# Kernel tuning notes

Measured on AMD Instinct MI355X. Metric: run time of the kernel, lower is better.

## Reference

```python
import jax, jax.numpy as jnp
import numpy as np


def _sage_layer(x_src, x_dst, src, dst, n_dst, W_neigh, W_self, b):
    # mean aggregation of src features onto dst nodes (zero for isolated dst)
    msgs = x_src[src]                                            # [E, d_in]
    summed = jax.ops.segment_sum(msgs, dst, num_segments=n_dst)  # [n_dst, d_in]
    deg = jax.ops.segment_sum(jnp.ones_like(dst, dtype=x_src.dtype), dst,
                              num_segments=n_dst)                # [n_dst]
    mean = summed / jnp.maximum(deg, 1)[:, None]
    # DGL SAGEConv('mean'): fc_self(h_dst) + fc_neigh(h_mean) + bias
    return x_dst @ W_self + mean @ W_neigh + b


def setup_inputs() -> dict:
    key = jax.random.key(0)
    ks = jax.random.split(key, 12)
    N_SRC, D_IN, HID, OUT = 100000, 128, 256, 64
    SIZE1, SIZE2 = 25000, 5000
    E1, E2 = 800000, 160000

    def glorot(k, shape):
        lim = np.sqrt(6.0 / (shape[0] + shape[1])).astype(np.float32)
        return jax.random.uniform(k, shape, jnp.float32, -lim, lim)

    return {
        "x": jax.random.normal(ks[0], (N_SRC, D_IN), jnp.float32),
        "W_self1": glorot(ks[1], (D_IN, HID)),
        "W_neigh1": glorot(ks[2], (D_IN, HID)),
        "b1": jnp.zeros((HID,), jnp.float32),
        "W_self2": glorot(ks[3], (HID, OUT)),
        "W_neigh2": glorot(ks[4], (HID, OUT)),
        "b2": jnp.zeros((OUT,), jnp.float32),
        "edge_src1": jax.random.randint(ks[5], (E1,), 0, N_SRC, jnp.int32),
        "edge_dst1": jax.random.randint(ks[6], (E1,), 0, SIZE1, jnp.int32),
        "edge_src2": jax.random.randint(ks[7], (E2,), 0, SIZE1, jnp.int32),
        "edge_dst2": jax.random.randint(ks[8], (E2,), 0, SIZE2, jnp.int32),
        "size1": SIZE1,
        "size2": SIZE2,
    }


def reference(x, W_self1, W_neigh1, b1, W_self2, W_neigh2, b2,
              edge_src1, edge_dst1, edge_src2, edge_dst2, size1, size2):
    # Layer 1: src = all nodes, dst = first size1 nodes
    h = _sage_layer(x, x[:size1], edge_src1, edge_dst1, size1,
                    W_neigh1, W_self1, b1)
    h = jax.nn.relu(h)  # dropout is identity in eval mode
    # Layer 2: src = layer-1 outputs (size1 nodes), dst = first size2 nodes
    h = _sage_layer(h, h[:size2], edge_src2, edge_dst2, size2,
                    W_neigh2, W_self2, b2)
    return jax.nn.log_softmax(h, axis=-1)
```

## Files before the change

kernel.cpp:

```cpp
#include <hip/hip_runtime.h>


constexpr int D_IN  = 128;
constexpr int HID   = 256;
constexpr int OUT_D = 64;
constexpr int SIZE1 = 25000;
constexpr int SIZE2 = 5000;
constexpr int SEGC  = 16;
constexpr int OVFS  = 48;
constexpr int ROW   = 8 * SEGC + OVFS;
constexpr int ECH   = 2048;

using bf16x8 = __attribute__((ext_vector_type(8))) short;
using f32x4  = __attribute__((ext_vector_type(4))) float;
using f32x2  = __attribute__((ext_vector_type(2))) float;

__device__ inline unsigned short f32_to_bf16_rne(float f) {
    unsigned u = __builtin_bit_cast(unsigned, f);
    u = (u + 0x7fffu + ((u >> 16) & 1u)) >> 16;
    return (unsigned short)u;
}
__device__ inline unsigned pack_bf16(float lo, float hi) {
    return (unsigned)f32_to_bf16_rne(lo) | ((unsigned)f32_to_bf16_rne(hi) << 16);
}
__device__ inline void add16(float* a, uint4 v) {
    const unsigned u[4] = {v.x, v.y, v.z, v.w};
#pragma unroll
    for (int i = 0; i < 4; ++i) {
        f32x2 f0 = __builtin_amdgcn_cvt_pk_f32_fp8(u[i], false);
        f32x2 f1 = __builtin_amdgcn_cvt_pk_f32_fp8(u[i], true);
        a[i * 4 + 0] += f0.x; a[i * 4 + 1] += f0.y;
        a[i * 4 + 2] += f1.x; a[i * 4 + 3] += f1.y;
    }
}

__device__ inline void fill_body(const int* __restrict__ es,
                                 const int* __restrict__ ed, int E, int base0,
                                 int* __restrict__ cnt, int* __restrict__ ovf,
                                 int* __restrict__ csr) {
    int xcc;
    asm volatile("s_getreg_b32 %0, hwreg(HW_REG_XCC_ID)" : "=s"(xcc));
    xcc &= 7;
#pragma unroll
    for (int j = 0; j < ECH / 256; ++j) {
        int e = base0 + j * 256;
        if (e < E) {
            int d = ed[e];
            int pos = atomicAdd(&cnt[d * 8 + xcc], 1);
            if (pos < SEGC) {
                csr[(long)d * ROW + xcc * SEGC + pos] = es[e];
            } else {
                int po = atomicAdd(&ovf[d], 1);
                if (po < OVFS) csr[(long)d * ROW + 8 * SEGC + po] = es[e];
            }
        }
    }
}

__global__ void megafuse(const int* __restrict__ es1, const int* __restrict__ ed1,
                         int E1, int* __restrict__ cnt1, int* __restrict__ ovf1,
                         int* __restrict__ csr1,
                         const float* __restrict__ x, unsigned* __restrict__ xbu,
                         unsigned* __restrict__ x8u, long n4,
                         const float* __restrict__ Ws1, const float* __restrict__ Wn1,
                         const float* __restrict__ Ws2, const float* __restrict__ Wn2,
                         unsigned short* __restrict__ Wt1,
                         unsigned short* __restrict__ Wt2,
                         int f1, int f2) {
    const int b = blockIdx.x;
    const int tid = threadIdx.x;
    if (b < f1) {
        fill_body(es1, ed1, E1, b * ECH + tid, cnt1, ovf1, csr1);
    } else if (b < f2) {
        long i0 = (long)(b - f1) * 512 + tid;
#pragma unroll
        for (int j = 0; j < 2; ++j) {
            long i = i0 + j * 256;
            if (i < n4) {
                float4 v = reinterpret_cast<const float4*>(x)[i];
                int p = __builtin_amdgcn_cvt_pk_fp8_f32(v.x, v.y, 0, false);
                p = __builtin_amdgcn_cvt_pk_fp8_f32(v.z, v.w, p, true);
                x8u[i] = (unsigned)p;
                if (i < (long)SIZE1 * (D_IN / 4)) {
                    uint2 o;
                    o.x = pack_bf16(v.x, v.y);
                    o.y = pack_bf16(v.z, v.w);
                    reinterpret_cast<uint2*>(xbu)[i] = o;
                }
            }
        }
    } else {
        int i = (b - f2) * 256 + tid;
        if (i < HID * (2 * D_IN)) {
            int n = i >> 8, k = i & 255;
            float v = (k < D_IN) ? Ws1[k * HID + n] : Wn1[(k - D_IN) * HID + n];
            Wt1[i] = f32_to_bf16_rne(v);
        } else {
            int j = i - HID * (2 * D_IN);
            if (j < OUT_D * (2 * HID)) {
                int n = j >> 9, k = j & 511;
                float v = (k < HID) ? Ws2[k * OUT_D + n] : Wn2[(k - HID) * OUT_D + n];
                Wt2[j] = f32_to_bf16_rne(v);
            }
        }
    }
}

template <int GL, bool FUSE>
__global__ void agg_pull6(const uint4* __restrict__ X4,
                          const int* __restrict__ csr,
                          const int* __restrict__ cnt,
                          const int* __restrict__ ovf,
                          uint4* __restrict__ meanOut, int ndst, int aggBlocks,
                          const int* __restrict__ esF, const int* __restrict__ edF,
                          int EF, int* __restrict__ cntF, int* __restrict__ ovfF,
                          int* __restrict__ csrF) {
    if (FUSE && (int)blockIdx.x >= aggBlocks) {
        fill_body(esF, edF, EF, ((int)blockIdx.x - aggBlocks) * ECH + threadIdx.x,
                  cntF, ovfF, csrF);
        return;
    }
    constexpr int NG = 64 / GL;
    constexpr int NR = (64 + NG * 8 - 1) / (NG * 8);
    const int wid = threadIdx.x >> 6;
    const int lane = threadIdx.x & 63;
    const int d = blockIdx.x * 4 + wid;
    if (d >= ndst) return;

    int myc = 0;
    if (lane < 8) myc = min(cnt[d * 8 + lane], SEGC);
    else if (lane == 8) myc = min(ovf[d], OVFS);
    int cum[10];
    cum[0] = 0;
#pragma unroll
    for (int k = 0; k < 9; ++k) cum[k + 1] = cum[k] + __shfl(myc, k);
    const int n = cum[9];
    const long rowb = (long)d * ROW;

    int slot = lane;
#pragma unroll
    for (int t = 1; t < 9; ++t)
        if (lane >= cum[t]) slot = (t < 8 ? t * SEGC : 8 * SEGC) + (lane - cum[t]);
    int myidx = 0;
    if (lane < n) myidx = csr[rowb + slot];

    const int g = lane / GL;
    const int c = lane % GL;
    const int nmain = min(n, 64);

    float acc[16];
#pragma unroll
    for (int j = 0; j < 16; ++j) acc[j] = 0.0f;

#pragma unroll
    for (int r = 0; r < NR; ++r) {
        const int base = r * NG * 8;
        if (base < nmain) {
            int s[8];
            bool act[8];
#pragma unroll
            for (int t = 0; t < 8; ++t) {
                const int e = base + g + NG * t;
                int ss = __shfl(myidx, e & 63);
                act[t] = (e < nmain);
                s[t] = act[t] ? ss : 0;
            }
            uint4 v[8];
#pragma unroll
            for (int t = 0; t < 8; ++t) v[t] = X4[(long)s[t] * GL + c];
#pragma unroll
            for (int t = 0; t < 8; ++t)
                if (act[t]) add16(acc, v[t]);
        }
    }
    for (int j2 = 64 + g; j2 < n; j2 += NG) {
        int sl = j2;
#pragma unroll
        for (int t = 1; t < 9; ++t)
            if (j2 >= cum[t]) sl = (t < 8 ? t * SEGC : 8 * SEGC) + (j2 - cum[t]);
        long s0 = csr[rowb + sl];
        uint4 v0 = X4[s0 * GL + c];
        add16(acc, v0);
    }
#pragma unroll
    for (int j = 0; j < 16; ++j) {
        if (GL == 8) acc[j] += __shfl_xor(acc[j], 8);
        acc[j] += __shfl_xor(acc[j], 16);
        acc[j] += __shfl_xor(acc[j], 32);
    }
    if (g == 0) {
        const float inv = 1.0f / (float)max(n, 1);
        uint4 o0, o1;
        o0.x = pack_bf16(acc[0] * inv, acc[1] * inv);
        o0.y = pack_bf16(acc[2] * inv, acc[3] * inv);
        o0.z = pack_bf16(acc[4] * inv, acc[5] * inv);
        o0.w = pack_bf16(acc[6] * inv, acc[7] * inv);
        o1.x = pack_bf16(acc[8] * inv, acc[9] * inv);
        o1.y = pack_bf16(acc[10] * inv, acc[11] * inv);
        o1.z = pack_bf16(acc[12] * inv, acc[13] * inv);
        o1.w = pack_bf16(acc[14] * inv, acc[15] * inv);
        meanOut[(long)d * (GL * 2) + c * 2]     = o0;
        meanOut[(long)d * (GL * 2) + c * 2 + 1] = o1;
    }
}

template <int KPH, bool RELU, bool OUT_BF16, bool LSM, bool H8>
__global__ __launch_bounds__(256) void sage_gemm_mfma(
    const unsigned short* __restrict__ Aself,
    const unsigned short* __restrict__ Amean,
    const unsigned short* __restrict__ Wt,
    const float* __restrict__ bias,
    void* __restrict__ Cout, unsigned char* __restrict__ H8out, int M, int N) {
    constexpr int BM = 64, BN = 64;
    constexpr int ITERS = (BM * KPH) / (256 * 8);
    __shared__ unsigned short As[BM * KPH];
    __shared__ unsigned short Bs[BN * KPH];

    const int tid = threadIdx.x;
    const int wid = tid >> 6;
    const int lane = tid & 63;
    const int wm = wid >> 1, wn = wid & 1;
    const int rowBase = blockIdx.x * BM;
    const int colBase = blockIdx.y * BN;

    f32x4 acc[2][2];
#pragma unroll
    for (int a = 0; a < 2; ++a)
#pragma unroll
        for (int b = 0; b < 2; ++b)
#pragma unroll
            for (int j = 0; j < 4; ++j) acc[a][b][j] = 0.0f;

#pragma unroll
    for (int p = 0; p < 2; ++p) {
        const unsigned short* __restrict__ A = p ? Amean : Aself;
        __syncthreads();
#pragma unroll
        for (int it = 0; it < ITERS; ++it) {
            int flat = (it * 256 + tid) * 8;
            int r = flat / KPH, kc = flat % KPH;
            int gr = rowBase + r;
            if (gr >= M) gr = M - 1;
            uint4 v = *reinterpret_cast<const uint4*>(&A[(long)gr * KPH + kc]);
            int idx = (r * KPH + kc) ^ ((r & 7) << 3);
            *reinterpret_cast<uint4*>(&As[idx]) = v;
        }
#pragma unroll
        for (int it = 0; it < ITERS; ++it) {
            int flat = (it * 256 + tid) * 8;
            int r = flat / KPH, kc = flat % KPH;
            uint4 v = *reinterpret_cast<const uint4*>(
                &Wt[(long)(colBase + r) * (2 * KPH) + p * KPH + kc]);
            int idx = (r * KPH + kc) ^ ((r & 7) << 3);
            *reinterpret_cast<uint4*>(&Bs[idx]) = v;
        }
        __syncthreads();
#pragma unroll
        for (int kk = 0; kk < KPH / 32; ++kk) {
            bf16x8 a[2], b[2];
            const int kb = kk * 32 + 8 * (lane >> 4);
#pragma unroll
            for (int f = 0; f < 2; ++f) {
                int r = wm * 32 + f * 16 + (lane & 15);
                int ia = (r * KPH + kb) ^ ((r & 7) << 3);
                a[f] = *reinterpret_cast<const bf16x8*>(&As[ia]);
                int rn = wn * 32 + f * 16 + (lane & 15);
                int ib = (rn * KPH + kb) ^ ((rn & 7) << 3);
                b[f] = *reinterpret_cast<const bf16x8*>(&Bs[ib]);
            }
#pragma unroll
            for (int fm = 0; fm < 2; ++fm)
#pragma unroll
                for (int fn = 0; fn < 2; ++fn)
                    acc[fm][fn] = __builtin_amdgcn_mfma_f32_16x16x32_bf16(
                        a[fm], b[fn], acc[fm][fn], 0, 0, 0);
        }
    }

    if (LSM) {
        float* sm = reinterpret_cast<float*>(As);
        __syncthreads();
#pragma unroll
        for (int fm = 0; fm < 2; ++fm)
#pragma unroll
            for (int fn = 0; fn < 2; ++fn) {
                int c = wn * 32 + fn * 16 + (lane & 15);
                float bv = bias[colBase + c];
#pragma unroll
                for (int j = 0; j < 4; ++j) {
                    int r = wm * 32 + fm * 16 + 4 * (lane >> 4) + j;
                    sm[r * BN + c] = acc[fm][fn][j] + bv;
                }
            }
        __syncthreads();
        for (int rr = 0; rr < 16; ++rr) {
            int r = wid * 16 + rr;
            int gr = rowBase + r;
            if (gr >= M) continue;
            float v = sm[r * BN + lane];
            float m = v;
#pragma unroll
            for (int o = 32; o; o >>= 1) m = fmaxf(m, __shfl_xor(m, o));
            float ex = __expf(v - m);
            float s = ex;
#pragma unroll
            for (int o = 32; o; o >>= 1) s += __shfl_xor(s, o);
            ((float*)Cout)[(long)gr * N + lane] = v - m - __logf(s);
        }
    } else {
#pragma unroll
        for (int fm = 0; fm < 2; ++fm) {
#pragma unroll
            for (int fn = 0; fn < 2; ++fn) {
                int gc = colBase + wn * 32 + fn * 16 + (lane & 15);
                float bv = bias[gc];
#pragma unroll
                for (int j = 0; j < 4; ++j) {
                    int gr = rowBase + wm * 32 + fm * 16 + 4 * (lane >> 4) + j;
                    if (gr < M) {
                        float v = acc[fm][fn][j] + bv;
                        if (RELU) v = fmaxf(v, 0.0f);
                        if (OUT_BF16)
                            ((unsigned short*)Cout)[(long)gr * N + gc] =
                                f32_to_bf16_rne(v);
                        else
                            ((float*)Cout)[(long)gr * N + gc] = v;
                        if (H8) {
                            int b8 = __builtin_amdgcn_cvt_pk_fp8_f32(v, v, 0, false);
                            H8out[(long)gr * N + gc] = (unsigned char)(b8 & 0xff);
                        }
                    }
                }
            }
        }
    }
}


extern "C" void kernel_launch(void* const* d_in, const int* in_sizes, int n_in,
                              void* d_out, int out_size, void* d_ws, size_t ws_size,
                              hipStream_t stream) {
    const float* x       = (const float*)d_in[0];
    const float* Wself1  = (const float*)d_in[1];
    const float* Wneigh1 = (const float*)d_in[2];
    const float* b1      = (const float*)d_in[3];
    const float* Wself2  = (const float*)d_in[4];
    const float* Wneigh2 = (const float*)d_in[5];
    const float* b2      = (const float*)d_in[6];
    const int* es1 = (const int*)d_in[7];
    const int* ed1 = (const int*)d_in[8];
    const int* es2 = (const int*)d_in[9];
    const int* ed2 = (const int*)d_in[10];
    const int E1 = in_sizes[7];
    const int E2 = in_sizes[9];
    const long NSRC = in_sizes[0] / D_IN;

    int* cnt1 = (int*)d_ws;
    int* ovf1 = cnt1 + (size_t)SIZE1 * 8;
    int* cnt2 = ovf1 + SIZE1;
    int* ovf2 = cnt2 + (size_t)SIZE2 * 8;
    int* csr2 = ovf2 + SIZE2;
    int* csr1 = csr2 + (size_t)SIZE2 * ROW;
    const size_t zero_ints = (size_t)SIZE1 * 9 + (size_t)SIZE2 * 9;
    const size_t int_elems = zero_ints + (size_t)SIZE2 * ROW + (size_t)SIZE1 * ROW;
    unsigned short* xb  = (unsigned short*)((int*)d_ws + int_elems);
    unsigned short* mean2 = xb;
    unsigned char* x8   = (unsigned char*)(xb + (size_t)SIZE1 * D_IN);
    unsigned short* Wt1 = (unsigned short*)(x8 + NSRC * D_IN);
    unsigned short* Wt2 = Wt1 + (size_t)HID * (2 * D_IN);
    unsigned short* mean1 = Wt2 + (size_t)OUT_D * (2 * HID);
    unsigned char* h8   = (unsigned char*)(mean1 + (size_t)SIZE1 * D_IN);
    unsigned short* h1  = (unsigned short*)csr1;

    hipMemsetAsync(d_ws, 0, zero_ints * sizeof(int), stream);

    const long n4 = NSRC * D_IN / 4;
    const int f1 = (E1 + ECH - 1) / ECH;
    const int f2 = f1 + (int)((n4 + 511) / 512);
    const int nb_cw = (HID * (2 * D_IN) + OUT_D * (2 * HID) + 255) / 256;
    megafuse<<<f2 + nb_cw, 256, 0, stream>>>(
        es1, ed1, E1, cnt1, ovf1, csr1,
        x, (unsigned*)xb, (unsigned*)x8, n4,
        Wself1, Wneigh1, Wself2, Wneigh2, Wt1, Wt2, f1, f2);

    {
        const int aggB = (SIZE1 + 3) / 4;
        const int fillB = (E2 + ECH - 1) / ECH;
        agg_pull6<8, true><<<aggB + fillB, 256, 0, stream>>>(
            (const uint4*)x8, csr1, cnt1, ovf1, (uint4*)mean1, SIZE1, aggB,
            es2, ed2, E2, cnt2, ovf2, csr2);
    }
    {
        dim3 grid((SIZE1 + 63) / 64, HID / 64);
        sage_gemm_mfma<D_IN, true, true, false, true><<<grid, 256, 0, stream>>>(
            xb, mean1, Wt1, b1, h1, h8, SIZE1, HID);
    }

    agg_pull6<16, false><<<(SIZE2 + 3) / 4, 256, 0, stream>>>(
        (const uint4*)h8, csr2, cnt2, ovf2, (uint4*)mean2, SIZE2, 1 << 30,
        nullptr, nullptr, 0, nullptr, nullptr, nullptr);
    {
        dim3 grid((SIZE2 + 63) / 64, OUT_D / 64);
        sage_gemm_mfma<HID, false, false, true, false><<<grid, 256, 0, stream>>>(
            h1, mean2, Wt2, b2, d_out, nullptr, SIZE2, OUT_D);
    }
}
```

Baseline: 129.9 us.

## Split megafuse into flat CSR fill and fp8 conversion, fuse bf16/weight conversion into aggregation

Replaces the combined fill/convert kernel with a dedicated one-edge-per-thread CSR fill covering both layers' edges and a separate fp8 conversion kernel. The bf16 conversion of the first SIZE1 rows and the weight transposes are moved into spare blocks of the layer-1 aggregation kernel, replacing the layer-2 fill that used to run there. The aim is to cut per-thread serial atomic work in the fill and to balance work across launches, at the cost of one extra kernel launch and a second read of x for the bf16 conversion.

```diff
diff --git a/kernel.cpp b/kernel.cpp
--- a/kernel.cpp
+++ b/kernel.cpp
@@ -9,7 +9,6 @@
 constexpr int SEGC  = 16;
 constexpr int OVFS  = 48;
 constexpr int ROW   = 8 * SEGC + OVFS;
-constexpr int ECH   = 2048;
 
 using bf16x8 = __attribute__((ext_vector_type(8))) short;
 using f32x4  = __attribute__((ext_vector_type(4))) float;
@@ -34,90 +33,97 @@
     }
 }
 
-__device__ inline void fill_body(const int* __restrict__ es,
-                                 const int* __restrict__ ed, int E, int base0,
-                                 int* __restrict__ cnt, int* __restrict__ ovf,
-                                 int* __restrict__ csr) {
+__global__ void fill_flat(const int* __restrict__ es1, const int* __restrict__ ed1,
+                          int E1, int* __restrict__ cnt1, int* __restrict__ ovf1,
+                          int* __restrict__ csr1,
+                          const int* __restrict__ es2, const int* __restrict__ ed2,
+                          int E2, int* __restrict__ cnt2, int* __restrict__ ovf2,
+                          int* __restrict__ csr2) {
     int xcc;
     asm volatile("s_getreg_b32 %0, hwreg(HW_REG_XCC_ID)" : "=s"(xcc));
     xcc &= 7;
-#pragma unroll
-    for (int j = 0; j < ECH / 256; ++j) {
-        int e = base0 + j * 256;
-        if (e < E) {
-            int d = ed[e];
-            int pos = atomicAdd(&cnt[d * 8 + xcc], 1);
-            if (pos < SEGC) {
-                csr[(long)d * ROW + xcc * SEGC + pos] = es[e];
-            } else {
-                int po = atomicAdd(&ovf[d], 1);
-                if (po < OVFS) csr[(long)d * ROW + 8 * SEGC + po] = es[e];
-            }
-        }
-    }
-}
-
-__global__ void megafuse(const int* __restrict__ es1, const int* __restrict__ ed1,
-                         int E1, int* __restrict__ cnt1, int* __restrict__ ovf1,
-                         int* __restrict__ csr1,
-                         const float* __restrict__ x, unsigned* __restrict__ xbu,
-                         unsigned* __restrict__ x8u, long n4,
-                         const float* __restrict__ Ws1, const float* __restrict__ Wn1,
-                         const float* __restrict__ Ws2, const float* __restrict__ Wn2,
-                         unsigned short* __restrict__ Wt1,
-                         unsigned short* __restrict__ Wt2,
-                         int f1, int f2) {
-    const int b = blockIdx.x;
-    const int tid = threadIdx.x;
-    if (b < f1) {
-        fill_body(es1, ed1, E1, b * ECH + tid, cnt1, ovf1, csr1);
-    } else if (b < f2) {
-        long i0 = (long)(b - f1) * 512 + tid;
-#pragma unroll
-        for (int j = 0; j < 2; ++j) {
-            long i = i0 + j * 256;
-            if (i < n4) {
-                float4 v = reinterpret_cast<const float4*>(x)[i];
-                int p = __builtin_amdgcn_cvt_pk_fp8_f32(v.x, v.y, 0, false);
-                p = __builtin_amdgcn_cvt_pk_fp8_f32(v.z, v.w, p, true);
-                x8u[i] = (unsigned)p;
+    const long i = (long)blockIdx.x * 256 + threadIdx.x;
+    if (i < E1) {
+        int d = ed1[i];
+        int pos = atomicAdd(&cnt1[d * 8 + xcc], 1);
+        if (pos < SEGC) {
+            csr1[(long)d * ROW + xcc * SEGC + pos] = es1[i];
+        } else {
+            int po = atomicAdd(&ovf1[d], 1);
+            if (po < OVFS) csr1[(long)d * ROW + 8 * SEGC + po] = es1[i];
+        }
+    } else if (i < (long)E1 + E2) {
+        int e = (int)(i - E1);
+        int d = ed2[e];
+        int pos = atomicAdd(&cnt2[d * 8 + xcc], 1);
+        if (pos < SEGC) {
+            csr2[(long)d * ROW + xcc * SEGC + pos] = es2[e];
+        } else {
+            int po = atomicAdd(&ovf2[d], 1);
+            if (po < OVFS) csr2[(long)d * ROW + 8 * SEGC + po] = es2[e];
+        }
+    }
+}
+
+__global__ void conv_x8(const float* __restrict__ x, unsigned* __restrict__ x8u,
+                        long n4) {
+    long i0 = (long)blockIdx.x * 512 + threadIdx.x;
+#pragma unroll
+    for (int j = 0; j < 2; ++j) {
+        long i = i0 + j * 256;
+        if (i < n4) {
+            float4 v = reinterpret_cast<const float4*>(x)[i];
+            int p = __builtin_amdgcn_cvt_pk_fp8_f32(v.x, v.y, 0, false);
+            p = __builtin_amdgcn_cvt_pk_fp8_f32(v.z, v.w, p, true);
+            x8u[i] = (unsigned)p;
+        }
+    }
+}
+
+template <int GL, bool CONV>
+__global__ void agg_pull7(const uint4* __restrict__ X4,
+                          const int* __restrict__ csr,
+                          const int* __restrict__ cnt,
+                          const int* __restrict__ ovf,
+                          uint4* __restrict__ meanOut, int ndst, int aggBlocks,
+                          const float* __restrict__ x, unsigned* __restrict__ xbu,
+                          const float* __restrict__ Ws1, const float* __restrict__ Wn1,
+                          const float* __restrict__ Ws2, const float* __restrict__ Wn2,
+                          unsigned short* __restrict__ Wt1,
+                          unsigned short* __restrict__ Wt2) {
+    if (CONV && (int)blockIdx.x >= aggBlocks) {
+        const int b = (int)blockIdx.x - aggBlocks;
+        const int tid = threadIdx.x;
+        constexpr int NB_XB = (SIZE1 * D_IN / 4 + 511) / 512;
+        if (b < NB_XB) {
+            long i0 = (long)b * 512 + tid;
+#pragma unroll
+            for (int j = 0; j < 2; ++j) {
+                long i = i0 + j * 256;
                 if (i < (long)SIZE1 * (D_IN / 4)) {
+                    float4 v = reinterpret_cast<const float4*>(x)[i];
                     uint2 o;
                     o.x = pack_bf16(v.x, v.y);
                     o.y = pack_bf16(v.z, v.w);
                     reinterpret_cast<uint2*>(xbu)[i] = o;
                 }
             }
-        }
-    } else {
-        int i = (b - f2) * 256 + tid;
-        if (i < HID * (2 * D_IN)) {
-            int n = i >> 8, k = i & 255;
-            float v = (k < D_IN) ? Ws1[k * HID + n] : Wn1[(k - D_IN) * HID + n];
-            Wt1[i] = f32_to_bf16_rne(v);
         } else {
-            int j = i - HID * (2 * D_IN);
-            if (j < OUT_D * (2 * HID)) {
-                int n = j >> 9, k = j & 511;
-                float v = (k < HID) ? Ws2[k * OUT_D + n] : Wn2[(k - HID) * OUT_D + n];
-                Wt2[j] = f32_to_bf16_rne(v);
-            }
-        }
-    }
-}
-
-template <int GL, bool FUSE>
-__global__ void agg_pull6(const uint4* __restrict__ X4,
-                          const int* __restrict__ csr,
-                          const int* __restrict__ cnt,
-                          const int* __restrict__ ovf,
-                          uint4* __restrict__ meanOut, int ndst, int aggBlocks,
-                          const int* __restrict__ esF, const int* __restrict__ edF,
-                          int EF, int* __restrict__ cntF, int* __restrict__ ovfF,
-                          int* __restrict__ csrF) {
-    if (FUSE && (int)blockIdx.x >= aggBlocks) {
-        fill_body(esF, edF, EF, ((int)blockIdx.x - aggBlocks) * ECH + threadIdx.x,
-                  cntF, ovfF, csrF);
+            int i = (b - NB_XB) * 256 + tid;
+            if (i < HID * (2 * D_IN)) {
+                int n = i >> 8, k = i & 255;
+                float v = (k < D_IN) ? Ws1[k * HID + n] : Wn1[(k - D_IN) * HID + n];
+                Wt1[i] = f32_to_bf16_rne(v);
+            } else {
+                int j = i - HID * (2 * D_IN);
+                if (j < OUT_D * (2 * HID)) {
+                    int n = j >> 9, k = j & 511;
+                    float v = (k < HID) ? Ws2[k * OUT_D + n]
+                                        : Wn2[(k - HID) * OUT_D + n];
+                    Wt2[j] = f32_to_bf16_rne(v);
+                }
+            }
+        }
         return;
     }
     constexpr int NG = 64 / GL;
@@ -374,31 +380,35 @@
 
     hipMemsetAsync(d_ws, 0, zero_ints * sizeof(int), stream);
 
+    {
+        const long tot = (long)E1 + E2;
+        fill_flat<<<(int)((tot + 255) / 256), 256, 0, stream>>>(
+            es1, ed1, E1, cnt1, ovf1, csr1,
+            es2, ed2, E2, cnt2, ovf2, csr2);
+    }
+
     const long n4 = NSRC * D_IN / 4;
-    const int f1 = (E1 + ECH - 1) / ECH;
-    const int f2 = f1 + (int)((n4 + 511) / 512);
-    const int nb_cw = (HID * (2 * D_IN) + OUT_D * (2 * HID) + 255) / 256;
-    megafuse<<<f2 + nb_cw, 256, 0, stream>>>(
-        es1, ed1, E1, cnt1, ovf1, csr1,
-        x, (unsigned*)xb, (unsigned*)x8, n4,
-        Wself1, Wneigh1, Wself2, Wneigh2, Wt1, Wt2, f1, f2);
+    conv_x8<<<(int)((n4 + 511) / 512), 256, 0, stream>>>(x, (unsigned*)x8, n4);
 
     {
         const int aggB = (SIZE1 + 3) / 4;
-        const int fillB = (E2 + ECH - 1) / ECH;
-        agg_pull6<8, true><<<aggB + fillB, 256, 0, stream>>>(
+        const int nb_xb = (SIZE1 * D_IN / 4 + 511) / 512;
+        const int nb_cw = (HID * (2 * D_IN) + OUT_D * (2 * HID) + 255) / 256;
+        agg_pull7<8, true><<<aggB + nb_xb + nb_cw, 256, 0, stream>>>(
             (const uint4*)x8, csr1, cnt1, ovf1, (uint4*)mean1, SIZE1, aggB,
-            es2, ed2, E2, cnt2, ovf2, csr2);
-    }
+            x, (unsigned*)xb, Wself1, Wneigh1, Wself2, Wneigh2, Wt1, Wt2);
+    }
+
     {
         dim3 grid((SIZE1 + 63) / 64, HID / 64);
         sage_gemm_mfma<D_IN, true, true, false, true><<<grid, 256, 0, stream>>>(
             xb, mean1, Wt1, b1, h1, h8, SIZE1, HID);
     }
 
-    agg_pull6<16, false><<<(SIZE2 + 3) / 4, 256, 0, stream>>>(
+    agg_pull7<16, false><<<(SIZE2 + 3) / 4, 256, 0, stream>>>(
         (const uint4*)h8, csr2, cnt2, ovf2, (uint4*)mean2, SIZE2, 1 << 30,
-        nullptr, nullptr, 0, nullptr, nullptr, nullptr);
+        nullptr, nullptr, nullptr, nullptr, nullptr, nullptr, nullptr, nullptr);
+
     {
         dim3 grid((SIZE2 + 63) / 64, OUT_D / 64);
         sage_gemm_mfma<HID, false, false, true, false><<<grid, 256, 0, stream>>>(
```

Measured after the change: 149.9 us. 15.4% more time.
